# Kernel optimization log

Hardware: AMD Instinct MI355X
Metric: run time of the kernel (lower is better)

The kernel has to match this reference:

```python
import jax, jax.numpy as jnp
import numpy as np


def setup_inputs() -> dict:
    key = jax.random.key(0)
    k1, k2, k3 = jax.random.split(key, 3)
    B, T, F = 32, 8192, 80
    ODIM, IDIM = 1024, 640
    src_tokens = jax.random.normal(k1, (B, T, F), dtype=jnp.float32)
    src_lengths = jax.random.randint(k2, (B,), 3, T + 1, dtype=jnp.int64)
    # xavier_normal_ on Linear weight [odim, idim]
    std = float(np.sqrt(2.0 / (ODIM + IDIM)))
    W = jax.random.normal(k3, (ODIM, IDIM), dtype=jnp.float32) * std
    b = jnp.zeros((ODIM,), dtype=jnp.float32)
    return {"src_tokens": src_tokens, "src_lengths": src_lengths, "W": W, "b": b}


def reference(src_tokens, src_lengths, W, b):
    B, T, F = src_tokens.shape
    n_frames = (T // 3) * 3
    out_lengths = src_lengths // 3 - 2
    # stack 3 consecutive frames: cat(x[:, ::3], x[:, 1::3], x[:, 2::3], -1) == reshape
    x = src_tokens[:, :n_frames, :].reshape(B, n_frames // 3, 3 * F)  # [B, M, 240]
    # window of 3 stacked frames -> feature 9F = 720, then keep first 640
    x = jnp.concatenate((x[:, :-2, :], x[:, 1:-1, :], x[:, 2:, :]), axis=-1)  # [B, M-2, 720]
    x = x[:, :, : x.shape[-1] - 80]  # [B, M-2, 640]
    x = jnp.transpose(x, (1, 0, 2))  # [T', B, 640]
    y = jnp.einsum("tbi,oi->tbo", x, W) + b  # [T', B, odim]
    # GLU on dim=1 (the batch dim, as in the original code)
    half = y.shape[1] // 2
    x_out = y[:, :half, :] * jax.nn.sigmoid(y[:, half:, :])  # [T', B/2, odim]
    return (x_out, out_lengths)
```

## Files before the change

kernel.cpp:

```cpp
#include <hip/hip_runtime.h>

#define GLOBAL_AS __attribute__((address_space(1)))
#define LDS_AS    __attribute__((address_space(3)))

typedef __bf16 bf16x8 __attribute__((ext_vector_type(8)));
typedef float  f32x4  __attribute__((ext_vector_type(4)));

constexpr int SRC_STRIDE = 8192 * 80;
constexpr int TOUT       = 2728;
constexpr long OUT_ELEMS = (long)TOUT * 16 * 1024;
constexpr int SRC_ELEMS  = 32 * SRC_STRIDE;
constexpr int W_ELEMS    = 1024 * 640;
constexpr int MBLK       = 682;

__device__ __forceinline__ unsigned short f2bf(float f) {
    union { float f; unsigned u; } a; a.f = f;
    unsigned r = a.u + 0x7FFF + ((a.u >> 16) & 1);
    return (unsigned short)(r >> 16);
}

__global__ void cvt_kernel(const float* __restrict__ in, unsigned short* __restrict__ out, int n4) {
    int i = blockIdx.x * blockDim.x + threadIdx.x;
    if (i >= n4) return;
    float4 v = ((const float4*)in)[i];
    ushort4 o;
    o.x = f2bf(v.x); o.y = f2bf(v.y); o.z = f2bf(v.z); o.w = f2bf(v.w);
    ((ushort4*)out)[i] = o;
}

__global__ void lengths_kernel(const int* __restrict__ len, float* __restrict__ out) {
    int i = threadIdx.x;
    if (i < 32) out[OUT_ELEMS + i] = (float)(len[i] / 3 - 2);
}

__global__ void glu_gemm(const __bf16* __restrict__ A,
                         const __bf16* __restrict__ Wb,
                         const float* __restrict__ bias,
                         float* __restrict__ out) {
    __shared__ __bf16 lA[128 * 64];
    __shared__ __bf16 lB[128 * 64];

    const int tid  = threadIdx.x;
    const int lane = tid & 63;
    const int w    = tid >> 6;
    const int wm   = w & 1;
    const int wn   = w >> 1;

    const int bid = blockIdx.x;
    const int bn  = (bid >> 3) & 7;
    const int bm  = (bid >> 6) * 8 + (bid & 7);
    if (bm >= MBLK) return;

    const int c8 = (((lane & 7) ^ (lane >> 3)) * 8);
    int aoff_g[4], boff_g[4];
#pragma unroll
    for (int j = 0; j < 4; ++j) {
        int r = w * 32 + j * 8 + (lane >> 3);
        int m = bm * 128 + r;
        int t = m >> 5, b = m & 31;
        aoff_g[j] = b * SRC_STRIDE + t * 240 + c8;
        int n = bn * 128 + r;
        boff_g[j] = n * 640 + c8;
    }

    const int q    = lane >> 4;
    const int poff = ((q ^ (lane & 7)) * 8);
    int aoff_l[4], boff_l[4];
#pragma unroll
    for (int i = 0; i < 4; ++i) {
        aoff_l[i] = (wm * 64 + i * 16 + (lane & 15)) * 64;
        boff_l[i] = (wn * 64 + i * 16 + (lane & 15)) * 64;
    }

    f32x4 acc[4][4] = {};

    for (int kb = 0; kb < 10; ++kb) {
        const int k0 = kb * 64;
#pragma unroll
        for (int j = 0; j < 4; ++j) {
            __builtin_amdgcn_global_load_lds(
                (const GLOBAL_AS void*)(A + (aoff_g[j] + k0)),
                (LDS_AS void*)(lA + (w * 32 + j * 8) * 64), 16, 0, 0);
            __builtin_amdgcn_global_load_lds(
                (const GLOBAL_AS void*)(Wb + (boff_g[j] + k0)),
                (LDS_AS void*)(lB + (w * 32 + j * 8) * 64), 16, 0, 0);
        }
        __syncthreads();
#pragma unroll
        for (int ks = 0; ks < 2; ++ks) {
            const int po = poff ^ (ks << 5);
            bf16x8 af[4], bfv[4];
#pragma unroll
            for (int i = 0; i < 4; ++i)
                af[i] = *(const bf16x8*)(lA + aoff_l[i] + po);
#pragma unroll
            for (int i = 0; i < 4; ++i)
                bfv[i] = *(const bf16x8*)(lB + boff_l[i] + po);
#pragma unroll
            for (int mt = 0; mt < 4; ++mt)
#pragma unroll
                for (int nt = 0; nt < 4; ++nt)
                    acc[mt][nt] = __builtin_amdgcn_mfma_f32_16x16x32_bf16(
                        af[mt], bfv[nt], acc[mt][nt], 0, 0, 0);
        }
        __syncthreads();
    }

    const int col = lane & 15;
    float bv[4];
#pragma unroll
    for (int nt = 0; nt < 4; ++nt)
        bv[nt] = bias[bn * 128 + wn * 64 + nt * 16 + col];

    const int t_base = bm * 4 + wm * 2;
#pragma unroll
    for (int pr = 0; pr < 2; ++pr) {
        const int t = t_base + pr;
#pragma unroll
        for (int nt = 0; nt < 4; ++nt) {
            const int n = bn * 128 + wn * 64 + nt * 16 + col;
#pragma unroll
            for (int r2 = 0; r2 < 4; ++r2) {
                const int brow = q * 4 + r2;
                float v = acc[pr * 2 + 0][nt][r2] + bv[nt];
                float g = acc[pr * 2 + 1][nt][r2] + bv[nt];
                float s = 1.0f / (1.0f + __expf(-g));
                out[((long)(t * 16 + brow)) * 1024 + n] = v * s;
            }
        }
    }
}

extern "C" void kernel_launch(void* const* d_in, const int* in_sizes, int n_in,
                              void* d_out, int out_size, void* d_ws, size_t ws_size,
                              hipStream_t stream) {
    const float* src  = (const float*)d_in[0];
    const int*   lens = (const int*)d_in[1];
    const float* Wf   = (const float*)d_in[2];
    const float* bias = (const float*)d_in[3];
    float* out = (float*)d_out;

    unsigned short* srcb = (unsigned short*)d_ws;
    unsigned short* wb   = srcb + SRC_ELEMS;

    cvt_kernel<<<SRC_ELEMS / 4 / 256, 256, 0, stream>>>(src, srcb, SRC_ELEMS / 4);
    cvt_kernel<<<W_ELEMS / 4 / 256, 256, 0, stream>>>(Wf, wb, W_ELEMS / 4);

    lengths_kernel<<<1, 64, 0, stream>>>(lens, out);

    glu_gemm<<<86 * 64, 256, 0, stream>>>((const __bf16*)srcb, (const __bf16*)wb, bias, out);
}
```

Baseline: 343.2 us.

## Enlarge GEMM tile to 256x256 with 4-stage async LDS pipeline

```diff
diff --git a/kernel.cpp b/kernel.cpp
--- a/kernel.cpp
+++ b/kernel.cpp
@@ -11,7 +11,9 @@
 constexpr long OUT_ELEMS = (long)TOUT * 16 * 1024;
 constexpr int SRC_ELEMS  = 32 * SRC_STRIDE;
 constexpr int W_ELEMS    = 1024 * 640;
-constexpr int MBLK       = 682;
+constexpr int MBLK       = 341;
+constexpr int NT         = 20;
+constexpr int SLOT       = 16384;
 
 __device__ __forceinline__ unsigned short f2bf(float f) {
     union { float f; unsigned u; } a; a.f = f;
@@ -33,97 +35,141 @@
     if (i < 32) out[OUT_ELEMS + i] = (float)(len[i] / 3 - 2);
 }
 
-__global__ void glu_gemm(const __bf16* __restrict__ A,
-                         const __bf16* __restrict__ Wb,
-                         const float* __restrict__ bias,
-                         float* __restrict__ out) {
-    __shared__ __bf16 lA[128 * 64];
-    __shared__ __bf16 lB[128 * 64];
+__global__ __launch_bounds__(512, 2)
+void glu_gemm(const __bf16* __restrict__ A,
+              const __bf16* __restrict__ Wb,
+              const float* __restrict__ bias,
+              float* __restrict__ out) {
+    __shared__ __bf16 lds[4 * SLOT];
 
     const int tid  = threadIdx.x;
     const int lane = tid & 63;
     const int w    = tid >> 6;
-    const int wm   = w & 1;
-    const int wn   = w >> 1;
+    const int wm   = w >> 2;
+    const int wn   = w & 3;
 
     const int bid = blockIdx.x;
-    const int bn  = (bid >> 3) & 7;
-    const int bm  = (bid >> 6) * 8 + (bid & 7);
+    const int bn  = (bid >> 3) & 3;
+    const int bm  = (bid >> 5) * 8 + (bid & 7);
     if (bm >= MBLK) return;
 
-    const int c8 = (((lane & 7) ^ (lane >> 3)) * 8);
-    int aoff_g[4], boff_g[4];
+    const int sl  = lane >> 3;
+    const int sp  = lane & 7;
+    const int sc  = sp ^ sl;
+    const int scc = (sc & 3) * 8;
+    const int srp = sc >> 2;
+    int aG[2], bG[2];
 #pragma unroll
-    for (int j = 0; j < 4; ++j) {
-        int r = w * 32 + j * 8 + (lane >> 3);
-        int m = bm * 128 + r;
-        int t = m >> 5, b = m & 31;
-        aoff_g[j] = b * SRC_STRIDE + t * 240 + c8;
-        int n = bn * 128 + r;
-        boff_g[j] = n * 640 + c8;
+    for (int h = 0; h < 2; ++h) {
+        int R = 2 * (h * 64 + w * 8 + sl) + srp;
+        int m = bm * 256 + R;
+        aG[h] = (m & 31) * SRC_STRIDE + (m >> 5) * 240 + scc;
+        int n = bn * 256 + R;
+        bG[h] = n * 640 + scc;
     }
+    const int aD0 = (w * 8) * 64;
+    const int aD1 = (64 + w * 8) * 64;
+    const int bD0 = 8192 + aD0;
+    const int bD1 = 8192 + aD1;
 
-    const int q    = lane >> 4;
-    const int poff = ((q ^ (lane & 7)) * 8);
-    int aoff_l[4], boff_l[4];
+    const int ll  = (lane & 15) >> 1;
+    const int pfr = (((lane & 1) << 2) | (lane >> 4)) ^ ll;
+    const int aB  = (wm * 64 + ll) * 64 + pfr * 8;
+    const int bB  = 8192 + (wn * 32 + ll) * 64 + pfr * 8;
+
+    f32x4 acc[8][4] = {};
+
 #pragma unroll
-    for (int i = 0; i < 4; ++i) {
-        aoff_l[i] = (wm * 64 + i * 16 + (lane & 15)) * 64;
-        boff_l[i] = (wn * 64 + i * 16 + (lane & 15)) * 64;
+    for (int t = 0; t < 3; ++t) {
+        const int so = t * SLOT;
+        const int kg = t * 32;
+        __builtin_amdgcn_global_load_lds((const GLOBAL_AS void*)(A + (aG[0] + kg)),
+                                         (LDS_AS void*)(lds + so + aD0), 16, 0, 0);
+        __builtin_amdgcn_global_load_lds((const GLOBAL_AS void*)(A + (aG[1] + kg)),
+                                         (LDS_AS void*)(lds + so + aD1), 16, 0, 0);
+        __builtin_amdgcn_global_load_lds((const GLOBAL_AS void*)(Wb + (bG[0] + kg)),
+                                         (LDS_AS void*)(lds + so + bD0), 16, 0, 0);
+        __builtin_amdgcn_global_load_lds((const GLOBAL_AS void*)(Wb + (bG[1] + kg)),
+                                         (LDS_AS void*)(lds + so + bD1), 16, 0, 0);
     }
+    asm volatile("s_waitcnt vmcnt(8)" ::: "memory");
+    __builtin_amdgcn_s_barrier();
 
-    f32x4 acc[4][4] = {};
+    for (int t = 0; t < NT; ++t) {
+        const int cur = (t & 3) * SLOT;
+        const int nxt = ((t + 3) & 3) * SLOT;
+        const int kg  = (t + 3) * 32;
+        const bool st = (t < NT - 3);
 
-    for (int kb = 0; kb < 10; ++kb) {
-        const int k0 = kb * 64;
+        bf16x8 af[4], bfv[4];
 #pragma unroll
-        for (int j = 0; j < 4; ++j) {
-            __builtin_amdgcn_global_load_lds(
-                (const GLOBAL_AS void*)(A + (aoff_g[j] + k0)),
-                (LDS_AS void*)(lA + (w * 32 + j * 8) * 64), 16, 0, 0);
-            __builtin_amdgcn_global_load_lds(
-                (const GLOBAL_AS void*)(Wb + (boff_g[j] + k0)),
-                (LDS_AS void*)(lB + (w * 32 + j * 8) * 64), 16, 0, 0);
+        for (int i = 0; i < 4; ++i)
+            af[i] = *(const bf16x8*)(lds + cur + aB + i * 512);
+#pragma unroll
+        for (int i = 0; i < 4; ++i)
+            bfv[i] = *(const bf16x8*)(lds + cur + bB + i * 512);
+        if (st) {
+            __builtin_amdgcn_global_load_lds((const GLOBAL_AS void*)(A + (aG[0] + kg)),
+                                             (LDS_AS void*)(lds + nxt + aD0), 16, 0, 0);
+            __builtin_amdgcn_global_load_lds((const GLOBAL_AS void*)(A + (aG[1] + kg)),
+                                             (LDS_AS void*)(lds + nxt + aD1), 16, 0, 0);
         }
-        __syncthreads();
+        __builtin_amdgcn_s_barrier();
+        __builtin_amdgcn_s_setprio(1);
 #pragma unroll
-        for (int ks = 0; ks < 2; ++ks) {
-            const int po = poff ^ (ks << 5);
-            bf16x8 af[4], bfv[4];
+        for (int mt = 0; mt < 4; ++mt)
 #pragma unroll
-            for (int i = 0; i < 4; ++i)
-                af[i] = *(const bf16x8*)(lA + aoff_l[i] + po);
+            for (int nt = 0; nt < 4; ++nt)
+                acc[mt][nt] = __builtin_amdgcn_mfma_f32_16x16x32_bf16(
+                    af[mt], bfv[nt], acc[mt][nt], 0, 0, 0);
+        __builtin_amdgcn_s_setprio(0);
+        __builtin_amdgcn_s_barrier();
+
+        bf16x8 ag[4];
 #pragma unroll
-            for (int i = 0; i < 4; ++i)
-                bfv[i] = *(const bf16x8*)(lB + boff_l[i] + po);
+        for (int i = 0; i < 4; ++i)
+            ag[i] = *(const bf16x8*)(lds + cur + aB + (i + 4) * 512);
+        if (st) {
+            __builtin_amdgcn_global_load_lds((const GLOBAL_AS void*)(Wb + (bG[0] + kg)),
+                                             (LDS_AS void*)(lds + nxt + bD0), 16, 0, 0);
+            __builtin_amdgcn_global_load_lds((const GLOBAL_AS void*)(Wb + (bG[1] + kg)),
+                                             (LDS_AS void*)(lds + nxt + bD1), 16, 0, 0);
+        }
+        __builtin_amdgcn_s_barrier();
+        __builtin_amdgcn_s_setprio(1);
 #pragma unroll
-            for (int mt = 0; mt < 4; ++mt)
+        for (int mt = 0; mt < 4; ++mt)
 #pragma unroll
-                for (int nt = 0; nt < 4; ++nt)
-                    acc[mt][nt] = __builtin_amdgcn_mfma_f32_16x16x32_bf16(
-                        af[mt], bfv[nt], acc[mt][nt], 0, 0, 0);
-        }
-        __syncthreads();
+            for (int nt = 0; nt < 4; ++nt)
+                acc[mt + 4][nt] = __builtin_amdgcn_mfma_f32_16x16x32_bf16(
+                    ag[mt], bfv[nt], acc[mt + 4][nt], 0, 0, 0);
+        __builtin_amdgcn_s_setprio(0);
+
+        if (t < NT - 3)       asm volatile("s_waitcnt vmcnt(8)" ::: "memory");
+        else if (t == NT - 3) asm volatile("s_waitcnt vmcnt(4)" ::: "memory");
+        else if (t == NT - 2) asm volatile("s_waitcnt vmcnt(0)" ::: "memory");
+        __builtin_amdgcn_s_barrier();
     }
 
     const int col = lane & 15;
-    float bv[4];
+    const int q   = lane >> 4;
+    float bvs[4];
 #pragma unroll
-    for (int nt = 0; nt < 4; ++nt)
-        bv[nt] = bias[bn * 128 + wn * 64 + nt * 16 + col];
+    for (int nf = 0; nf < 4; ++nf)
+        bvs[nf] = bias[bn * 256 + wn * 64 + nf * 16 + col];
 
-    const int t_base = bm * 4 + wm * 2;
+    const int tb = bm * 8 + wm * 4;
 #pragma unroll
-    for (int pr = 0; pr < 2; ++pr) {
-        const int t = t_base + pr;
+    for (int i = 0; i < 4; ++i) {
+        const int t = tb + i;
 #pragma unroll
-        for (int nt = 0; nt < 4; ++nt) {
-            const int n = bn * 128 + wn * 64 + nt * 16 + col;
+        for (int nf = 0; nf < 4; ++nf) {
+            const int n = bn * 256 + wn * 64 + nf * 16 + col;
 #pragma unroll
             for (int r2 = 0; r2 < 4; ++r2) {
                 const int brow = q * 4 + r2;
-                float v = acc[pr * 2 + 0][nt][r2] + bv[nt];
-                float g = acc[pr * 2 + 1][nt][r2] + bv[nt];
+                float v = acc[2 * i][nf][r2] + bvs[nf];
+                float g = acc[2 * i + 1][nf][r2] + bvs[nf];
                 float s = 1.0f / (1.0f + __expf(-g));
                 out[((long)(t * 16 + brow)) * 1024 + n] = v * s;
             }
@@ -148,5 +194,5 @@
 
     lengths_kernel<<<1, 64, 0, stream>>>(lens, out);
 
-    glu_gemm<<<86 * 64, 256, 0, stream>>>((const __bf16*)srcb, (const __bf16*)wb, bias, out);
+    glu_gemm<<<43 * 32, 512, 0, stream>>>((const __bf16*)srcb, (const __bf16*)wb, bias, out);
 }
```

New measurement: 367.0 us. 7.0% more time.

## Triple-buffer GEMM K-tiles in LDS with async global_load_lds prefetch

Applied to the files above, without the earlier changes.

```diff
diff --git a/kernel.cpp b/kernel.cpp
--- a/kernel.cpp
+++ b/kernel.cpp
@@ -12,6 +12,8 @@
 constexpr int SRC_ELEMS  = 32 * SRC_STRIDE;
 constexpr int W_ELEMS    = 1024 * 640;
 constexpr int MBLK       = 682;
+constexpr int NTILE      = 20;
+constexpr int SLOTE      = 8192;
 
 __device__ __forceinline__ unsigned short f2bf(float f) {
     union { float f; unsigned u; } a; a.f = f;
@@ -33,12 +35,23 @@
     if (i < 32) out[OUT_ELEMS + i] = (float)(len[i] / 3 - 2);
 }
 
-__global__ void glu_gemm(const __bf16* __restrict__ A,
-                         const __bf16* __restrict__ Wb,
-                         const float* __restrict__ bias,
-                         float* __restrict__ out) {
-    __shared__ __bf16 lA[128 * 64];
-    __shared__ __bf16 lB[128 * 64];
+#define GLD(gp, lp) __builtin_amdgcn_global_load_lds((const GLOBAL_AS void*)(gp), \
+                                                     (LDS_AS void*)(lp), 16, 0, 0)
+
+#define STAGE_T(tile_, soE_) do {                               \
+    const int kg_ = (tile_) * 32;                               \
+    GLD(A  + (aG[0] + kg_), lds + (soE_) + aD0);                \
+    GLD(A  + (aG[1] + kg_), lds + (soE_) + aD1);                \
+    GLD(Wb + (bG[0] + kg_), lds + (soE_) + bD0);                \
+    GLD(Wb + (bG[1] + kg_), lds + (soE_) + bD1);                \
+} while (0)
+
+__global__ __launch_bounds__(256, 3)
+void glu_gemm(const __bf16* __restrict__ A,
+              const __bf16* __restrict__ Wb,
+              const float* __restrict__ bias,
+              float* __restrict__ out) {
+    __shared__ __bf16 lds[3 * SLOTE];
 
     const int tid  = threadIdx.x;
     const int lane = tid & 63;
@@ -51,59 +64,86 @@
     const int bm  = (bid >> 6) * 8 + (bid & 7);
     if (bm >= MBLK) return;
 
-    const int c8 = (((lane & 7) ^ (lane >> 3)) * 8);
-    int aoff_g[4], boff_g[4];
+    const int sl  = lane >> 3;
+    const int sp  = lane & 7;
+    const int sc  = sp ^ sl;
+    const int scc = (sc & 3) * 8;
+    const int srp = sc >> 2;
+    int aG[2], bG[2];
 #pragma unroll
-    for (int j = 0; j < 4; ++j) {
-        int r = w * 32 + j * 8 + (lane >> 3);
-        int m = bm * 128 + r;
-        int t = m >> 5, b = m & 31;
-        aoff_g[j] = b * SRC_STRIDE + t * 240 + c8;
-        int n = bn * 128 + r;
-        boff_g[j] = n * 640 + c8;
+    for (int h = 0; h < 2; ++h) {
+        int R = 2 * (h * 32 + w * 8 + sl) + srp;
+        int m = bm * 128 + R;
+        aG[h] = (m & 31) * SRC_STRIDE + (m >> 5) * 240 + scc;
+        int n = bn * 128 + R;
+        bG[h] = n * 640 + scc;
     }
+    const int aD0 = (w * 8) * 64;
+    const int aD1 = (32 + w * 8) * 64;
+    const int bD0 = 4096 + aD0;
+    const int bD1 = 4096 + aD1;
 
-    const int q    = lane >> 4;
-    const int poff = ((q ^ (lane & 7)) * 8);
-    int aoff_l[4], boff_l[4];
-#pragma unroll
-    for (int i = 0; i < 4; ++i) {
-        aoff_l[i] = (wm * 64 + i * 16 + (lane & 15)) * 64;
-        boff_l[i] = (wn * 64 + i * 16 + (lane & 15)) * 64;
-    }
+    const int q   = lane >> 4;
+    const int ll  = (lane & 15) >> 1;
+    const int pfr = (((lane & 1) << 2) | q) ^ ll;
+    const int aB  = (wm * 32 + ll) * 64 + pfr * 8;
+    const int bB  = 4096 + (wn * 32 + ll) * 64 + pfr * 8;
+
+    const unsigned LB    = (unsigned)(unsigned long long)(&lds[0]);
+    const unsigned adrA0 = LB + 2u * (unsigned)aB;
+    const unsigned adrB0 = LB + 2u * (unsigned)bB;
 
     f32x4 acc[4][4] = {};
 
-    for (int kb = 0; kb < 10; ++kb) {
-        const int k0 = kb * 64;
+    unsigned curE = 0, nxtE = SLOTE, prvE = 2 * SLOTE;
+
+    STAGE_T(0, 0);
+    STAGE_T(1, SLOTE);
+    __builtin_amdgcn_sched_barrier(0);
+    asm volatile("s_waitcnt vmcnt(4)");
+    __builtin_amdgcn_sched_barrier(0);
+    __builtin_amdgcn_s_barrier();
+
+#pragma unroll 1
+    for (int t = 0; t < NTILE; ++t) {
+        if (t < NTILE - 2) STAGE_T(t + 2, prvE);
+
+        const unsigned aAdr = adrA0 + 2u * curE;
+        const unsigned bAdr = adrB0 + 2u * curE;
+        bf16x8 af0, af1, af2, af3, bf0, bf1, bf2, bf3;
+        asm volatile("ds_read_b128 %0, %1 offset:0"    : "=v"(af0) : "v"(aAdr));
+        asm volatile("ds_read_b128 %0, %1 offset:1024" : "=v"(af1) : "v"(aAdr));
+        asm volatile("ds_read_b128 %0, %1 offset:2048" : "=v"(af2) : "v"(aAdr));
+        asm volatile("ds_read_b128 %0, %1 offset:3072" : "=v"(af3) : "v"(aAdr));
+        asm volatile("ds_read_b128 %0, %1 offset:0"    : "=v"(bf0) : "v"(bAdr));
+        asm volatile("ds_read_b128 %0, %1 offset:1024" : "=v"(bf1) : "v"(bAdr));
+        asm volatile("ds_read_b128 %0, %1 offset:2048" : "=v"(bf2) : "v"(bAdr));
+        asm volatile("ds_read_b128 %0, %1 offset:3072" : "=v"(bf3) : "v"(bAdr));
+        __builtin_amdgcn_sched_barrier(0);
+        asm volatile("s_waitcnt lgkmcnt(0)");
+        __builtin_amdgcn_sched_barrier(0);
+
+        __builtin_amdgcn_s_setprio(1);
 #pragma unroll
-        for (int j = 0; j < 4; ++j) {
-            __builtin_amdgcn_global_load_lds(
-                (const GLOBAL_AS void*)(A + (aoff_g[j] + k0)),
-                (LDS_AS void*)(lA + (w * 32 + j * 8) * 64), 16, 0, 0);
-            __builtin_amdgcn_global_load_lds(
-                (const GLOBAL_AS void*)(Wb + (boff_g[j] + k0)),
-                (LDS_AS void*)(lB + (w * 32 + j * 8) * 64), 16, 0, 0);
+        for (int mt = 0; mt < 4; ++mt) {
+            acc[mt][0] = __builtin_amdgcn_mfma_f32_16x16x32_bf16(
+                (mt==0?af0:mt==1?af1:mt==2?af2:af3), bf0, acc[mt][0], 0, 0, 0);
+            acc[mt][1] = __builtin_amdgcn_mfma_f32_16x16x32_bf16(
+                (mt==0?af0:mt==1?af1:mt==2?af2:af3), bf1, acc[mt][1], 0, 0, 0);
+            acc[mt][2] = __builtin_amdgcn_mfma_f32_16x16x32_bf16(
+                (mt==0?af0:mt==1?af1:mt==2?af2:af3), bf2, acc[mt][2], 0, 0, 0);
+            acc[mt][3] = __builtin_amdgcn_mfma_f32_16x16x32_bf16(
+                (mt==0?af0:mt==1?af1:mt==2?af2:af3), bf3, acc[mt][3], 0, 0, 0);
         }
-        __syncthreads();
-#pragma unroll
-        for (int ks = 0; ks < 2; ++ks) {
-            const int po = poff ^ (ks << 5);
-            bf16x8 af[4], bfv[4];
-#pragma unroll
-            for (int i = 0; i < 4; ++i)
-                af[i] = *(const bf16x8*)(lA + aoff_l[i] + po);
-#pragma unroll
-            for (int i = 0; i < 4; ++i)
-                bfv[i] = *(const bf16x8*)(lB + boff_l[i] + po);
-#pragma unroll
-            for (int mt = 0; mt < 4; ++mt)
-#pragma unroll
-                for (int nt = 0; nt < 4; ++nt)
-                    acc[mt][nt] = __builtin_amdgcn_mfma_f32_16x16x32_bf16(
-                        af[mt], bfv[nt], acc[mt][nt], 0, 0, 0);
-        }
-        __syncthreads();
+        __builtin_amdgcn_s_setprio(0);
+        __builtin_amdgcn_sched_barrier(0);
+
+        if (t < NTILE - 2)       { asm volatile("s_waitcnt vmcnt(4)"); }
+        else if (t == NTILE - 2) { asm volatile("s_waitcnt vmcnt(0)"); }
+        __builtin_amdgcn_sched_barrier(0);
+        if (t < NTILE - 1) __builtin_amdgcn_s_barrier();
+
+        const unsigned tmp = prvE; prvE = curE; curE = nxtE; nxtE = tmp;
     }
 
     const int col = lane & 15;
```

New measurement: 371.9 us. +8.4%, slower.
